# Optimization experiments

Hardware: AMD Instinct MI355X
Metric: run time of the kernel (lower is better)

Reference implementation:

```python
import jax, jax.numpy as jnp
import numpy as np

F_LEN = 21          # function_length
D_LEN = 41          # distribution_length
SLOPE = 1.0         # function_slope (nonzero -> tanh branch)
EPS = 1e-12         # torch F.normalize eps


def setup_inputs() -> dict:
    key = jax.random.key(0)
    k1, k2, k3, k4, k5 = jax.random.split(key, 5)
    B, L = 64, 2048
    S = F_LEN + D_LEN - 1  # 61, segment length required by the sliding slices
    lines_feature = jax.random.normal(k1, (B, L, 16), dtype=jnp.float32)
    pf = jax.random.uniform(k2, (B, L, S), dtype=jnp.float32, minval=0.1, maxval=1.0)
    pb = jax.random.uniform(k3, (B, L, S), dtype=jnp.float32, minval=0.1, maxval=1.0)
    slop = jax.random.uniform(k4, (B, L), dtype=jnp.float32, minval=0.5, maxval=2.5)
    amp = jax.random.uniform(k5, (B, L), dtype=jnp.float32, minval=0.1, maxval=0.4)
    return {
        "lines_feature": lines_feature,
        "lines_image_pf_segments": pf,
        "lines_image_pb_segments": pb,
        "lines_slop": slop,
        "lines_amplitude": amp,
    }


def reference(lines_feature, lines_image_pf_segments, lines_image_pb_segments,
              lines_slop, lines_amplitude):
    # lookup functions f/b over the function window  [B, L, F]
    x = jnp.arange(F_LEN, dtype=jnp.float32) - (F_LEN - 1) / 2.0
    lf = 0.5 - lines_amplitude[..., None] * jnp.tanh(x / (2.0 * lines_slop[..., None]))
    lb = 1.0 - lf

    # minimum variance floor (Laplace vs Gaussian)
    min_var_laplace = 1.0 / (2.0 * jnp.square(jnp.arctanh(2.0 * lines_amplitude)))
    min_var = jnp.maximum(min_var_laplace, lines_slop)

    # all D_LEN overlapping windows of length F_LEN, gathered in one shot
    idx = jnp.arange(D_LEN)[:, None] + jnp.arange(F_LEN)[None, :]   # [D, F]
    pf_win = lines_image_pf_segments[..., idx]                      # [B, L, D, F]
    pb_win = lines_image_pb_segments[..., idx]                      # [B, L, D, F]

    # log-domain product reduction over the window
    logp = jnp.log(pf_win * lf[..., None, :] + pb_win * lb[..., None, :]).sum(-1)
    dist = jnp.exp(logp)                                            # [B, L, D]

    # L1 normalize (torch.nn.functional.normalize, p=1)
    dist = dist / jnp.maximum(jnp.sum(jnp.abs(dist), axis=-1, keepdims=True), EPS)

    # line_distribution_extractor is identity pass-through of the distributions

    # Gaussian moment fit
    step = jnp.arange(D_LEN, dtype=jnp.float32)                     # [D]
    mean_tmp = jnp.sum(step * dist, axis=-1)                        # [B, L]
    var_tmp = jnp.sum(jnp.square(step - mean_tmp[..., None]) * dist, axis=-1)
    mean = mean_tmp - (D_LEN - 1) / 2.0
    var = jnp.maximum(var_tmp, min_var)
    return dist, mean, 1.0 / var
```

## Files before the change

### kernel.cpp

```cpp
#include <hip/hip_runtime.h>
#include <math.h>

#define F_LEN 21
#define D_LEN 41
#define S_LEN 61
#define ROWS 32
#define TPR 8
#define THREADS 256
#define PITCH 63
#define NELEM (ROWS * S_LEN)

__global__ __launch_bounds__(THREADS, 4) void bp_kernel(
    const float* __restrict__ pf_g, const float* __restrict__ pb_g,
    const float* __restrict__ slop_g, const float* __restrict__ amp_g,
    float* __restrict__ out_dist, float* __restrict__ out_mean,
    float* __restrict__ out_ivar)
{
    __shared__ float lds_f[ROWS * PITCH];
    __shared__ float lds_b[ROWS * PITCH];

    const int tid  = threadIdx.x;
    const int rl   = tid >> 3;
    const int q    = tid & 7;
    const int row0 = blockIdx.x * ROWS;
    const int r    = row0 + rl;

    #pragma unroll
    for (int it = 0; it < 8; ++it) {
        int idx = it * THREADS + tid;
        if (idx < NELEM) {
            int lr = idx / S_LEN;
            int s  = idx - lr * S_LEN;
            size_t g = (size_t)row0 * S_LEN + idx;
            lds_f[lr * PITCH + s] = pf_g[g];
            lds_b[lr * PITCH + s] = pb_g[g];
        }
    }

    const float a  = amp_g[r];
    const float sl = slop_g[r];

    float lf[F_LEN];
    lf[10] = 0.5f;
    {
        const float E = __expf(1.0f / sl);
        float Ek = 1.0f;
        #pragma unroll
        for (int k = 1; k <= 10; ++k) {
            Ek *= E;
            float t = __fdividef(Ek - 1.0f, Ek + 1.0f);
            float dl = a * t;
            lf[10 + k] = 0.5f - dl;
            lf[10 - k] = 0.5f + dl;
        }
    }

    __syncthreads();

    const int  d0    = q * 5;
    const bool has6  = (q == 7);
    const int  base  = rl * PITCH + d0;

    float prod[6] = {1.0f, 1.0f, 1.0f, 1.0f, 1.0f, 1.0f};
    #pragma unroll
    for (int i = 0; i < 26; ++i) {
        float f  = lds_f[base + i];
        float b  = lds_b[base + i];
        float df = f - b;
        #pragma unroll
        for (int dp = 0; dp < 6; ++dp) {
            const int j = i - dp;
            if (j >= 0 && j < F_LEN) {
                float t = fmaf(lf[j], df, b);
                if (dp == 5) t = has6 ? t : 1.0f;
                prod[dp] *= t;
            }
        }
    }

    const float df0 = (float)d0;
    float s0 = 0.0f, s1 = 0.0f, s2 = 0.0f;
    #pragma unroll
    for (int dp = 0; dp < 6; ++dp) {
        float p = prod[dp];
        if (dp == 5) p = has6 ? p : 0.0f;
        float dv = df0 + (float)dp;
        s0 += p;
        s1 += dv * p;
        s2 += dv * dv * p;
    }
    #pragma unroll
    for (int w = 1; w < 8; w <<= 1) {
        s0 += __shfl_xor(s0, w, 64);
        s1 += __shfl_xor(s1, w, 64);
        s2 += __shfl_xor(s2, w, 64);
    }

    const float inv      = 1.0f / fmaxf(s0, 1e-12f);
    const float mean_tmp = s1 * inv;
    const float m2       = s2 * inv;
    const float var_tmp  = fmaf(-mean_tmp, mean_tmp, m2);

    const float two_a = 2.0f * a;
    const float at    = 0.5f * logf((1.0f + two_a) / (1.0f - two_a));
    const float min_v = fmaxf(0.5f / (at * at), sl);
    const float var   = fmaxf(var_tmp, min_v);

    if (q == 0) {
        out_mean[r] = mean_tmp - (float)((D_LEN - 1) / 2);
        out_ivar[r] = 1.0f / var;
    }

    const size_t ob = (size_t)r * D_LEN + d0;
    #pragma unroll
    for (int dp = 0; dp < 5; ++dp)
        out_dist[ob + dp] = prod[dp] * inv;
    if (has6)
        out_dist[ob + 5] = prod[5] * inv;
}

extern "C" void kernel_launch(void* const* d_in, const int* in_sizes, int n_in,
                              void* d_out, int out_size, void* d_ws, size_t ws_size,
                              hipStream_t stream) {
    const float* pf   = (const float*)d_in[1];
    const float* pb   = (const float*)d_in[2];
    const float* slop = (const float*)d_in[3];
    const float* amp  = (const float*)d_in[4];

    const int rows = in_sizes[3];

    float* out_dist = (float*)d_out;
    float* out_mean = out_dist + (size_t)rows * D_LEN;
    float* out_ivar = out_mean + rows;

    const int blocks = rows / ROWS;
    bp_kernel<<<blocks, THREADS, 0, stream>>>(pf, pb, slop, amp,
                                              out_dist, out_mean, out_ivar);
}
```

Before: 28.61 us.

## Vectorize global loads/stores via float4 and interleave pf/pb in LDS

Global loads of the pf/pb segments now use float4 reads (the block's 32x61 tile is contiguous and divisible by 4), and the two arrays are interleaved into one float2 LDS array so each window step does one 8-byte LDS read. The scattered per-thread scalar stores of the distribution are replaced by staging through LDS and writing the block's contiguous 32x41 output with coalesced float4 stores. This cuts load/store instruction count and improves coalescing, at the cost of extra barriers. The unpadded stride-61 float2 layout may add LDS bank conflicts.

Measured after the change: 26.99 us. -5.7%, faster.

```diff
diff --git a/kernel.cpp b/kernel.cpp
--- a/kernel.cpp
+++ b/kernel.cpp
@@ -5,10 +5,11 @@
 #define D_LEN 41
 #define S_LEN 61
 #define ROWS 32
-#define TPR 8
 #define THREADS 256
-#define PITCH 63
 #define NELEM (ROWS * S_LEN)
+#define NV4   (NELEM / 4)
+#define DOUT  (ROWS * D_LEN)
+#define DV4   (DOUT / 4)
 
 __global__ __launch_bounds__(THREADS, 4) void bp_kernel(
     const float* __restrict__ pf_g, const float* __restrict__ pb_g,
@@ -16,8 +17,7 @@
     float* __restrict__ out_dist, float* __restrict__ out_mean,
     float* __restrict__ out_ivar)
 {
-    __shared__ float lds_f[ROWS * PITCH];
-    __shared__ float lds_b[ROWS * PITCH];
+    __shared__ float2 lds_fb[NELEM];
 
     const int tid  = threadIdx.x;
     const int rl   = tid >> 3;
@@ -25,15 +25,18 @@
     const int row0 = blockIdx.x * ROWS;
     const int r    = row0 + rl;
 
+    const float4* pf4 = (const float4*)(pf_g + (size_t)row0 * S_LEN);
+    const float4* pb4 = (const float4*)(pb_g + (size_t)row0 * S_LEN);
     #pragma unroll
-    for (int it = 0; it < 8; ++it) {
-        int idx = it * THREADS + tid;
-        if (idx < NELEM) {
-            int lr = idx / S_LEN;
-            int s  = idx - lr * S_LEN;
-            size_t g = (size_t)row0 * S_LEN + idx;
-            lds_f[lr * PITCH + s] = pf_g[g];
-            lds_b[lr * PITCH + s] = pb_g[g];
+    for (int it = 0; it < 2; ++it) {
+        int idx4 = it * THREADS + tid;
+        if (idx4 < NV4) {
+            float4 f = pf4[idx4];
+            float4 b = pb4[idx4];
+            lds_fb[idx4 * 4 + 0] = make_float2(f.x, b.x);
+            lds_fb[idx4 * 4 + 1] = make_float2(f.y, b.y);
+            lds_fb[idx4 * 4 + 2] = make_float2(f.z, b.z);
+            lds_fb[idx4 * 4 + 3] = make_float2(f.w, b.w);
         }
     }
 
@@ -57,21 +60,20 @@
 
     __syncthreads();
 
-    const int  d0    = q * 5;
-    const bool has6  = (q == 7);
-    const int  base  = rl * PITCH + d0;
+    const int  d0   = q * 5;
+    const bool has6 = (q == 7);
+    const int  base = rl * S_LEN + d0;
 
     float prod[6] = {1.0f, 1.0f, 1.0f, 1.0f, 1.0f, 1.0f};
     #pragma unroll
     for (int i = 0; i < 26; ++i) {
-        float f  = lds_f[base + i];
-        float b  = lds_b[base + i];
-        float df = f - b;
+        float2 fb = lds_fb[base + i];
+        float  df = fb.x - fb.y;
         #pragma unroll
         for (int dp = 0; dp < 6; ++dp) {
             const int j = i - dp;
             if (j >= 0 && j < F_LEN) {
-                float t = fmaf(lf[j], df, b);
+                float t = fmaf(lf[j], df, fb.y);
                 if (dp == 5) t = has6 ? t : 1.0f;
                 prod[dp] *= t;
             }
@@ -111,12 +113,22 @@
         out_ivar[r] = 1.0f / var;
     }
 
-    const size_t ob = (size_t)r * D_LEN + d0;
+    __syncthreads();
+    float* ldsd = (float*)lds_fb;
     #pragma unroll
     for (int dp = 0; dp < 5; ++dp)
-        out_dist[ob + dp] = prod[dp] * inv;
+        ldsd[rl * D_LEN + d0 + dp] = prod[dp] * inv;
     if (has6)
-        out_dist[ob + 5] = prod[5] * inv;
+        ldsd[rl * D_LEN + 40] = prod[5] * inv;
+    __syncthreads();
+
+    const float4* ld4 = (const float4*)ldsd;
+    float4* o4 = (float4*)(out_dist + (size_t)row0 * D_LEN);
+    #pragma unroll
+    for (int it = 0; it < 2; ++it) {
+        int idx4 = it * THREADS + tid;
+        if (idx4 < DV4) o4[idx4] = ld4[idx4];
+    }
 }
 
 extern "C" void kernel_launch(void* const* d_in, const int* in_sizes, int n_in,
```

## Process four row tiles per block with register-prefetched double-buffered LDS

Applied to the files above, without the earlier changes.

Each block now handles four 32-row tiles. It prefetches the next tile's pf/pb into registers with float4 loads while computing the current tile, then stages them into an alternating interleaved float2 LDS buffer. Distribution outputs are staged in LDS and written back with coalesced float4 stores. The aim is to overlap global loads with compute and to vectorize memory traffic. The cost is four times fewer blocks (1024 instead of 4096), extra LDS, and two barriers per tile.

Measured after the change: 49.86 us. 74.3% more time.

```diff
diff --git a/kernel.cpp b/kernel.cpp
--- a/kernel.cpp
+++ b/kernel.cpp
@@ -5,10 +5,19 @@
 #define D_LEN 41
 #define S_LEN 61
 #define ROWS 32
-#define TPR 8
 #define THREADS 256
-#define PITCH 63
+#define TILES 4
 #define NELEM (ROWS * S_LEN)
+#define NV4   (NELEM / 4)
+#define DOUT  (ROWS * D_LEN)
+#define DV4   (DOUT / 4)
+
+__device__ __forceinline__ void stage_write(float2* dst, float4 f, float4 b, int idx4) {
+    dst[idx4 * 4 + 0] = make_float2(f.x, b.x);
+    dst[idx4 * 4 + 1] = make_float2(f.y, b.y);
+    dst[idx4 * 4 + 2] = make_float2(f.z, b.z);
+    dst[idx4 * 4 + 3] = make_float2(f.w, b.w);
+}
 
 __global__ __launch_bounds__(THREADS, 4) void bp_kernel(
     const float* __restrict__ pf_g, const float* __restrict__ pb_g,
@@ -16,107 +25,134 @@
     float* __restrict__ out_dist, float* __restrict__ out_mean,
     float* __restrict__ out_ivar)
 {
-    __shared__ float lds_f[ROWS * PITCH];
-    __shared__ float lds_b[ROWS * PITCH];
+    __shared__ float2 buf[2][NELEM];
+    __shared__ float  distL[DOUT];
 
     const int tid  = threadIdx.x;
     const int rl   = tid >> 3;
     const int q    = tid & 7;
-    const int row0 = blockIdx.x * ROWS;
-    const int r    = row0 + rl;
+    const int tid2 = tid + 256;
+    const int brow = blockIdx.x * (TILES * ROWS);
+
+    float4 f0, f1, b0, b1;
+    float  aC, slC, aN, slN;
+
+    {
+        const float4* pf4 = (const float4*)(pf_g + (size_t)brow * S_LEN);
+        const float4* pb4 = (const float4*)(pb_g + (size_t)brow * S_LEN);
+        f0 = pf4[tid];  b0 = pb4[tid];
+        if (tid2 < NV4) { f1 = pf4[tid2]; b1 = pb4[tid2]; }
+        aC  = amp_g[brow + rl];
+        slC = slop_g[brow + rl];
+        stage_write(buf[0], f0, b0, tid);
+        if (tid2 < NV4) stage_write(buf[0], f1, b1, tid2);
+    }
+    __syncthreads();
 
     #pragma unroll
-    for (int it = 0; it < 8; ++it) {
-        int idx = it * THREADS + tid;
-        if (idx < NELEM) {
-            int lr = idx / S_LEN;
-            int s  = idx - lr * S_LEN;
-            size_t g = (size_t)row0 * S_LEN + idx;
-            lds_f[lr * PITCH + s] = pf_g[g];
-            lds_b[lr * PITCH + s] = pb_g[g];
+    for (int t = 0; t < TILES; ++t) {
+        const int row0 = brow + t * ROWS;
+        const int r    = row0 + rl;
+
+        if (t + 1 < TILES) {
+            const float4* pf4 = (const float4*)(pf_g + (size_t)(row0 + ROWS) * S_LEN);
+            const float4* pb4 = (const float4*)(pb_g + (size_t)(row0 + ROWS) * S_LEN);
+            f0 = pf4[tid];  b0 = pb4[tid];
+            if (tid2 < NV4) { f1 = pf4[tid2]; b1 = pb4[tid2]; }
+            aN  = amp_g[r + ROWS];
+            slN = slop_g[r + ROWS];
         }
-    }
 
-    const float a  = amp_g[r];
-    const float sl = slop_g[r];
+        float lf[F_LEN];
+        lf[10] = 0.5f;
+        {
+            const float E = __expf(1.0f / slC);
+            float Ek = 1.0f;
+            #pragma unroll
+            for (int k = 1; k <= 10; ++k) {
+                Ek *= E;
+                float tnh = __fdividef(Ek - 1.0f, Ek + 1.0f);
+                float dl  = aC * tnh;
+                lf[10 + k] = 0.5f - dl;
+                lf[10 - k] = 0.5f + dl;
+            }
+        }
 
-    float lf[F_LEN];
-    lf[10] = 0.5f;
-    {
-        const float E = __expf(1.0f / sl);
-        float Ek = 1.0f;
+        const float2* fb = buf[t & 1];
+        const int  d0    = q * 5;
+        const bool has6  = (q == 7);
+        const int  base  = rl * S_LEN + d0;
+
+        float prod[6] = {1.0f, 1.0f, 1.0f, 1.0f, 1.0f, 1.0f};
         #pragma unroll
-        for (int k = 1; k <= 10; ++k) {
-            Ek *= E;
-            float t = __fdividef(Ek - 1.0f, Ek + 1.0f);
-            float dl = a * t;
-            lf[10 + k] = 0.5f - dl;
-            lf[10 - k] = 0.5f + dl;
+        for (int i = 0; i < 26; ++i) {
+            float2 v  = fb[base + i];
+            float  df = v.x - v.y;
+            #pragma unroll
+            for (int dp = 0; dp < 6; ++dp) {
+                const int j = i - dp;
+                if (j >= 0 && j < F_LEN) {
+                    float tm = fmaf(lf[j], df, v.y);
+                    if (dp == 5) tm = has6 ? tm : 1.0f;
+                    prod[dp] *= tm;
+                }
+            }
         }
-    }
 
-    __syncthreads();
-
-    const int  d0    = q * 5;
-    const bool has6  = (q == 7);
-    const int  base  = rl * PITCH + d0;
-
-    float prod[6] = {1.0f, 1.0f, 1.0f, 1.0f, 1.0f, 1.0f};
-    #pragma unroll
-    for (int i = 0; i < 26; ++i) {
-        float f  = lds_f[base + i];
-        float b  = lds_b[base + i];
-        float df = f - b;
+        float s0 = 0.0f, s1 = 0.0f, s2 = 0.0f;
+        const float df0 = (float)d0;
         #pragma unroll
         for (int dp = 0; dp < 6; ++dp) {
-            const int j = i - dp;
-            if (j >= 0 && j < F_LEN) {
-                float t = fmaf(lf[j], df, b);
-                if (dp == 5) t = has6 ? t : 1.0f;
-                prod[dp] *= t;
-            }
+            float p = prod[dp];
+            if (dp == 5) p = has6 ? p : 0.0f;
+            float dv = df0 + (float)dp;
+            s0 += p;
+            s1 += dv * p;
+            s2 += dv * dv * p;
         }
+        #pragma unroll
+        for (int w = 1; w < 8; w <<= 1) {
+            s0 += __shfl_xor(s0, w, 64);
+            s1 += __shfl_xor(s1, w, 64);
+            s2 += __shfl_xor(s2, w, 64);
+        }
+
+        const float inv      = 1.0f / fmaxf(s0, 1e-12f);
+        const float mean_tmp = s1 * inv;
+        const float m2       = s2 * inv;
+        const float var_tmp  = fmaf(-mean_tmp, mean_tmp, m2);
+
+        const float two_a = 2.0f * aC;
+        const float at    = 0.5f * logf((1.0f + two_a) / (1.0f - two_a));
+        const float min_v = fmaxf(0.5f / (at * at), slC);
+        const float var   = fmaxf(var_tmp, min_v);
+
+        if (q == 0) {
+            out_mean[r] = mean_tmp - (float)((D_LEN - 1) / 2);
+            out_ivar[r] = 1.0f / var;
+        }
+
+        #pragma unroll
+        for (int dp = 0; dp < 5; ++dp)
+            distL[rl * D_LEN + d0 + dp] = prod[dp] * inv;
+        if (has6)
+            distL[rl * D_LEN + 40] = prod[5] * inv;
+
+        if (t + 1 < TILES) {
+            stage_write(buf[(t + 1) & 1], f0, b0, tid);
+            if (tid2 < NV4) stage_write(buf[(t + 1) & 1], f1, b1, tid2);
+            aC = aN; slC = slN;
+        }
+        __syncthreads();
+
+        {
+            const float4* ld4 = (const float4*)distL;
+            float4* o4 = (float4*)(out_dist + (size_t)row0 * D_LEN);
+            o4[tid] = ld4[tid];
+            if (tid2 < DV4) o4[tid2] = ld4[tid2];
+        }
+        __syncthreads();
     }
-
-    const float df0 = (float)d0;
-    float s0 = 0.0f, s1 = 0.0f, s2 = 0.0f;
-    #pragma unroll
-    for (int dp = 0; dp < 6; ++dp) {
-        float p = prod[dp];
-        if (dp == 5) p = has6 ? p : 0.0f;
-        float dv = df0 + (float)dp;
-        s0 += p;
-        s1 += dv * p;
-        s2 += dv * dv * p;
-    }
-    #pragma unroll
-    for (int w = 1; w < 8; w <<= 1) {
-        s0 += __shfl_xor(s0, w, 64);
-        s1 += __shfl_xor(s1, w, 64);
-        s2 += __shfl_xor(s2, w, 64);
-    }
-
-    const float inv      = 1.0f / fmaxf(s0, 1e-12f);
-    const float mean_tmp = s1 * inv;
-    const float m2       = s2 * inv;
-    const float var_tmp  = fmaf(-mean_tmp, mean_tmp, m2);
-
-    const float two_a = 2.0f * a;
-    const float at    = 0.5f * logf((1.0f + two_a) / (1.0f - two_a));
-    const float min_v = fmaxf(0.5f / (at * at), sl);
-    const float var   = fmaxf(var_tmp, min_v);
-
-    if (q == 0) {
-        out_mean[r] = mean_tmp - (float)((D_LEN - 1) / 2);
-        out_ivar[r] = 1.0f / var;
-    }
-
-    const size_t ob = (size_t)r * D_LEN + d0;
-    #pragma unroll
-    for (int dp = 0; dp < 5; ++dp)
-        out_dist[ob + dp] = prod[dp] * inv;
-    if (has6)
-        out_dist[ob + 5] = prod[5] * inv;
 }
 
 extern "C" void kernel_launch(void* const* d_in, const int* in_sizes, int n_in,
@@ -133,7 +169,7 @@
     float* out_mean = out_dist + (size_t)rows * D_LEN;
     float* out_ivar = out_mean + rows;
 
-    const int blocks = rows / ROWS;
+    const int blocks = rows / (ROWS * TILES);
     bp_kernel<<<blocks, THREADS, 0, stream>>>(pf, pb, slop, amp,
                                               out_dist, out_mean, out_ivar);
 }
```
